# Optimization experiments

Hardware: AMD Instinct MI355X
Metric: run time of the kernel (lower is better)

## Reference

```python
import jax, jax.numpy as jnp
import numpy as np

NUM_HEAD = 16
HEAD_DIM = 64
SEQ, BATCH, DMODEL = 2048, 2, 1024


def setup_inputs() -> dict:
    key = jax.random.key(0)
    ks = jax.random.split(key, 6)
    xavier = lambda k, shp: jax.random.uniform(
        k, shp, jnp.float32, -1.0, 1.0) * np.sqrt(6.0 / (shp[0] + shp[1]))
    query = jax.random.normal(ks[0], (SEQ, BATCH, DMODEL), jnp.float32)
    q_w = xavier(ks[1], (DMODEL, DMODEL))
    k_w = xavier(ks[2], (DMODEL, DMODEL))
    v_w = xavier(ks[3], (DMODEL, DMODEL))
    out_w = xavier(ks[4], (DMODEL, DMODEL))
    zeros = jnp.zeros((DMODEL,), jnp.float32)
    # causal mask: True = masked out (key position after query position)
    causal = jnp.triu(jnp.ones((SEQ, SEQ), bool), k=1)
    attn_mask = jnp.broadcast_to(causal, (BATCH, SEQ, SEQ))
    return {
        "query": query,
        "q_w": q_w, "q_b": zeros,
        "k_w": k_w, "k_b": zeros,
        "v_w": v_w, "v_b": zeros,
        "out_w": out_w, "out_b": zeros,
        "attn_mask": attn_mask,
    }


def reference(query, q_w, q_b, k_w, k_b, v_w, v_b, out_w, out_b, attn_mask):
    S, B, _ = query.shape
    H, Dh = NUM_HEAD, HEAD_DIM
    scale = 1.0 / np.sqrt(Dh)
    # self-attention: key = value = query
    q = (query @ q_w.T + q_b).reshape(S, B, H, Dh)
    k = (query @ k_w.T + k_b).reshape(S, B, H, Dh)
    v = (query @ v_w.T + v_b).reshape(S, B, H, Dh)
    # scores: [B, H, S(query), S(key)]
    scores = jnp.einsum('sbhd,tbhd->bhst', q, k) * scale
    scores = jnp.where(attn_mask[:, None, :, :], -jnp.inf, scores)
    attn = jax.nn.softmax(scores, axis=-1)
    # context: [S, B, H, Dh] -> [S, B, H*Dh]
    ctx = jnp.einsum('bhst,tbhd->sbhd', attn, v).reshape(S, B, H * Dh)
    return ctx @ out_w.T + out_b
```

## Files before the change

kernel.cpp:

```cpp
#include <hip/hip_runtime.h>
#include <hip/hip_bf16.h>

typedef __bf16 bf16;
typedef __attribute__((ext_vector_type(2))) __bf16 bf16x2;
typedef __attribute__((ext_vector_type(4))) __bf16 bf16x4;
typedef __attribute__((ext_vector_type(8))) __bf16 bf16x8;
typedef __attribute__((ext_vector_type(4))) float f32x4;

static_assert(sizeof(bf16x8) == 16, "bf16x8 must be 16B");

#define S_LEN 2048
#define BATCH_N 2
#define DM 1024
#define NHEAD 16
#define HDIM 64
#define LOG2E 1.44269504088896f

__device__ __forceinline__ void async_cp16(const void* g, void* l) {
    __builtin_amdgcn_global_load_lds(
        (const __attribute__((address_space(1))) void*)g,
        (__attribute__((address_space(3))) void*)l, 16, 0, 0);
}

__global__ __launch_bounds__(256)
void cvt_all(const float* __restrict__ q,
             const float* __restrict__ w0, const float* __restrict__ w1,
             const float* __restrict__ w2, const float* __restrict__ w3,
             bf16* __restrict__ Xb,
             bf16* __restrict__ W0, bf16* __restrict__ W1,
             bf16* __restrict__ W2, bf16* __restrict__ W3) {
    const int blk = blockIdx.x;
    const float* src;
    bf16* dst;
    size_t base;
    if (blk < 2048) {
        src = q; dst = Xb; base = (size_t)blk * 2048;
    } else {
        const int w = (blk - 2048) >> 9;
        const int r = (blk - 2048) & 511;
        base = (size_t)r * 2048;
        src = (w == 0) ? w0 : (w == 1) ? w1 : (w == 2) ? w2 : w3;
        dst = (w == 0) ? W0 : (w == 1) ? W1 : (w == 2) ? W2 : W3;
    }
    const size_t i = base + (size_t)threadIdx.x * 8;
    const f32x4 a = *(const f32x4*)(src + i);
    const f32x4 b = *(const f32x4*)(src + i + 4);
    bf16x8 r8;
    r8[0] = (bf16)a[0]; r8[1] = (bf16)a[1]; r8[2] = (bf16)a[2]; r8[3] = (bf16)a[3];
    r8[4] = (bf16)b[0]; r8[5] = (bf16)b[1]; r8[6] = (bf16)b[2]; r8[7] = (bf16)b[3];
    *(bf16x8*)(dst + i) = r8;
}

__device__ __forceinline__ void gemm_tile(const bf16* __restrict__ A,
                                          const bf16* __restrict__ W,
                                          int row0, int col0, int Kdim,
                                          f32x4 acc[4][4]) {
    __shared__ bf16 As[128 * 32];
    __shared__ bf16 Bs[128 * 32];
    const int tid  = threadIdx.x;
    const int lane = tid & 63;
    const int wv   = tid >> 6;
    const int wr = wv >> 1, wc = wv & 1;
    const int qr = lane & 15, quad = lane >> 4;

    const int srow = wv * 16 + (lane >> 2);
    const int scol = (lane & 3) * 8;
    const bf16* Ap = A + (size_t)(row0 + srow) * Kdim + scol;
    const bf16* Wp = W + (size_t)(col0 + srow) * Kdim + scol;
    bf16* lA0 = As + wv * 512;
    bf16* lA1 = As + 64 * 32 + wv * 512;
    bf16* lB0 = Bs + wv * 512;
    bf16* lB1 = Bs + 64 * 32 + wv * 512;

    const f32x4 fzero = {0.f, 0.f, 0.f, 0.f};
    #pragma unroll
    for (int mi = 0; mi < 4; ++mi)
        #pragma unroll
        for (int ni = 0; ni < 4; ++ni)
            acc[mi][ni] = fzero;

    for (int k0 = 0; k0 < Kdim; k0 += 32) {
        __syncthreads();
        async_cp16(Ap + k0, lA0);
        async_cp16(Ap + (size_t)64 * Kdim + k0, lA1);
        async_cp16(Wp + k0, lB0);
        async_cp16(Wp + (size_t)64 * Kdim + k0, lB1);
        __syncthreads();

        bf16x8 af[4], bfr[4];
        #pragma unroll
        for (int mi = 0; mi < 4; ++mi)
            af[mi] = *(const bf16x8*)(As + (wr * 64 + mi * 16 + qr) * 32 + quad * 8);
        #pragma unroll
        for (int ni = 0; ni < 4; ++ni)
            bfr[ni] = *(const bf16x8*)(Bs + (wc * 64 + ni * 16 + qr) * 32 + quad * 8);
        #pragma unroll
        for (int mi = 0; mi < 4; ++mi)
            #pragma unroll
            for (int ni = 0; ni < 4; ++ni)
                acc[mi][ni] = __builtin_amdgcn_mfma_f32_16x16x32_bf16(
                    af[mi], bfr[ni], acc[mi][ni], 0, 0, 0);
    }
}

__global__ __launch_bounds__(256)
void qkv_kernel(const bf16* __restrict__ X,
                const bf16* __restrict__ Wq, const float* __restrict__ bq,
                const bf16* __restrict__ Wk, const float* __restrict__ bk,
                const bf16* __restrict__ Wv, const float* __restrict__ bv,
                bf16* __restrict__ Q, bf16* __restrict__ Kt, bf16* __restrict__ Vt) {
    const int mat  = blockIdx.z;
    const bf16*  W    = (mat == 0) ? Wq : (mat == 1) ? Wk : Wv;
    const float* bias = (mat == 0) ? bq : (mat == 1) ? bk : bv;
    const int col0 = blockIdx.x * 128;
    const int row0 = blockIdx.y * 128;

    f32x4 acc[4][4];
    gemm_tile(X, W, row0, col0, DM, acc);

    const int lane = threadIdx.x & 63;
    const int wave = threadIdx.x >> 6;
    const int wr = wave >> 1, wc = wave & 1;
    const int qr = lane & 15, quad = lane >> 4;

    #pragma unroll
    for (int ni = 0; ni < 4; ++ni) {
        const int n  = col0 + wc * 64 + ni * 16 + qr;
        const float bn = bias[n];
        const int h = n >> 6, dh = n & 63;
        #pragma unroll
        for (int mi = 0; mi < 4; ++mi) {
            const int i0 = row0 + wr * 64 + mi * 16 + quad * 4;
            const float v0 = acc[mi][ni][0] + bn;
            const float v1 = acc[mi][ni][1] + bn;
            const float v2 = acc[mi][ni][2] + bn;
            const float v3 = acc[mi][ni][3] + bn;
            if (mat == 2) {
                const int s0 = i0 >> 1;
                bf16x2 e0 = {(bf16)v0, (bf16)v2};
                bf16x2 e1 = {(bf16)v1, (bf16)v3};
                *(bf16x2*)(Vt + ((size_t)h * HDIM + dh) * S_LEN + s0) = e0;
                *(bf16x2*)(Vt + ((size_t)(NHEAD + h) * HDIM + dh) * S_LEN + s0) = e1;
            } else {
                #pragma unroll
                for (int r = 0; r < 4; ++r) {
                    const int i = i0 + r;
                    const int s = i >> 1, b = i & 1;
                    const float v = (r == 0) ? v0 : (r == 1) ? v1 : (r == 2) ? v2 : v3;
                    if (mat == 0) {
                        Q[((size_t)(b * NHEAD + h) * S_LEN + s) * HDIM + dh] =
                            (bf16)(v * (0.125f * LOG2E));
                    } else {
                        Kt[((size_t)(b * NHEAD + h) * S_LEN + s) * HDIM + dh] = (bf16)v;
                    }
                }
            }
        }
    }
}

#define PLD 40
#define PT  640

#define MFMA(a, b, c) __builtin_amdgcn_mfma_f32_16x16x32_bf16(a, b, c, 0, 0, 0)
#define EX(x) __builtin_amdgcn_exp2f(x)

__global__ __launch_bounds__(256)
void attn_part(const bf16* __restrict__ Q, const bf16* __restrict__ K,
               const bf16* __restrict__ Vt, bf16* __restrict__ ctx) {
    __shared__ __align__(16) char smem[21504];
    const int tid  = threadIdx.x;
    const int lane = tid & 63;
    const int wave = tid >> 6;
    const int qr = lane & 15, quad = lane >> 4;
    const int bh = blockIdx.x & 31;
    const int bx = blockIdx.x >> 5;
    const int b = bh >> 4, h = bh & 15;

    const char* Kg = (const char*)(K  + (size_t)bh * S_LEN * HDIM);
    const char* Vg = (const char*)(Vt + (size_t)bh * HDIM * S_LEN);
    const bf16* Qb = Q + (size_t)bh * S_LEN * HDIM;
    char* Ksm = smem;
    char* Vsm = smem + 8192;
    bf16* Pw  = (bf16*)(smem + 16384) + wave * PT;
    const f32x4 fzero = {0.f, 0.f, 0.f, 0.f};

    const int qb     = 31 - bx;
    const int qb0    = qb * 64;
    const int tdiag  = qb * 2;
    const int ntiles = 2 * qb + 2;

    const int d16   = tid * 16;
    const int ksrow = d16 >> 7;
    const int ksoff = (d16 & 127) ^ ((ksrow & 7) << 4);
    const int vsrow = d16 >> 6;
    const int vsoff = (d16 & 63) ^ ((vsrow & 3) << 4);
    const size_t kgbase = (size_t)ksrow * 128 + ksoff;
    const size_t vgbase = (size_t)vsrow * (S_LEN * 2) + vsoff;

#define STAGE(t_, bi_) do { \
    async_cp16(Kg + (size_t)(t_) * 4096 + kgbase, Ksm + (bi_) * 4096 + wave * 1024); \
    async_cp16(Vg + (size_t)(t_) * 64   + vgbase, Vsm + (bi_) * 4096 + wave * 1024); \
} while (0)

    const int qrow0 = qb0 + wave * 16;
    const bf16x8 qlo = *(const bf16x8*)(Qb + (size_t)(qrow0 + qr) * HDIM + quad * 8);
    const bf16x8 qhi = *(const bf16x8*)(Qb + (size_t)(qrow0 + qr) * HDIM + quad * 8 + 32);

    f32x4 o0 = fzero, o1 = fzero, o2 = fzero, o3 = fzero;
    float l = 0.f;

    STAGE(0, 0);
    __syncthreads();

    const int sK = (qr & 7) << 4;
    const int sV = (qr & 3) << 4;

    for (int t = 0; t < ntiles; ++t) {
        const int cur = t & 1;
        if (t + 1 < ntiles) STAGE(t + 1, cur ^ 1);

        const char* Kc = Ksm + cur * 4096;
        const char* Vc = Vsm + cur * 4096;
        const bf16x8 k0 = *(const bf16x8*)(Kc + qr * 128        + ((quad * 16)      ^ sK));
        const bf16x8 k1 = *(const bf16x8*)(Kc + qr * 128        + ((quad * 16 + 64) ^ sK));
        const bf16x8 k2 = *(const bf16x8*)(Kc + (16 + qr) * 128 + ((quad * 16)      ^ sK));
        const bf16x8 k3 = *(const bf16x8*)(Kc + (16 + qr) * 128 + ((quad * 16 + 64) ^ sK));
        const bf16x8 v0 = *(const bf16x8*)(Vc + qr * 64         + ((quad * 16) ^ sV));
        const bf16x8 v1 = *(const bf16x8*)(Vc + (16 + qr) * 64  + ((quad * 16) ^ sV));
        const bf16x8 v2 = *(const bf16x8*)(Vc + (32 + qr) * 64  + ((quad * 16) ^ sV));
        const bf16x8 v3 = *(const bf16x8*)(Vc + (48 + qr) * 64  + ((quad * 16) ^ sV));

        f32x4 sA = MFMA(k0, qlo, fzero); sA = MFMA(k1, qhi, sA);
        f32x4 sB = MFMA(k2, qlo, fzero); sB = MFMA(k3, qhi, sB);

        if (t < tdiag) {
            const float e0 = EX(sA[0]), e1 = EX(sA[1]), e2 = EX(sA[2]), e3 = EX(sA[3]);
            const float f0 = EX(sB[0]), f1 = EX(sB[1]), f2 = EX(sB[2]), f3 = EX(sB[3]);
            l += (e0 + e1 + e2 + e3) + (f0 + f1 + f2 + f3);
            bf16x4 wa = {(bf16)e0, (bf16)e1, (bf16)e2, (bf16)e3};
            bf16x4 wb = {(bf16)f0, (bf16)f1, (bf16)f2, (bf16)f3};
            *(bf16x4*)(Pw + qr * PLD + quad * 4)      = wa;
            *(bf16x4*)(Pw + qr * PLD + 16 + quad * 4) = wb;
        } else {
            const int qrow = qrow0 + qr;
            const int ka = t * 32 + quad * 4;
            const float e0 = (ka + 0  <= qrow) ? EX(sA[0]) : 0.f;
            const float e1 = (ka + 1  <= qrow) ? EX(sA[1]) : 0.f;
            const float e2 = (ka + 2  <= qrow) ? EX(sA[2]) : 0.f;
            const float e3 = (ka + 3  <= qrow) ? EX(sA[3]) : 0.f;
            const float f0 = (ka + 16 <= qrow) ? EX(sB[0]) : 0.f;
            const float f1 = (ka + 17 <= qrow) ? EX(sB[1]) : 0.f;
            const float f2 = (ka + 18 <= qrow) ? EX(sB[2]) : 0.f;
            const float f3 = (ka + 19 <= qrow) ? EX(sB[3]) : 0.f;
            l += (e0 + e1 + e2 + e3) + (f0 + f1 + f2 + f3);
            bf16x4 wa = {(bf16)e0, (bf16)e1, (bf16)e2, (bf16)e3};
            bf16x4 wb = {(bf16)f0, (bf16)f1, (bf16)f2, (bf16)f3};
            *(bf16x4*)(Pw + qr * PLD + quad * 4)      = wa;
            *(bf16x4*)(Pw + qr * PLD + 16 + quad * 4) = wb;
        }

        const bf16x8 pf = *(const bf16x8*)(Pw + qr * PLD + quad * 8);
        __builtin_amdgcn_s_setprio(1);
        o0 = MFMA(v0, pf, o0); o1 = MFMA(v1, pf, o1);
        o2 = MFMA(v2, pf, o2); o3 = MFMA(v3, pf, o3);
        __builtin_amdgcn_s_setprio(0);

        __syncthreads();
    }
#undef STAGE

    l += __shfl_xor(l, 16); l += __shfl_xor(l, 32);
    const float n = 1.f / l;

    const int s_ = qrow0 + qr;
    bf16* cp = ctx + ((size_t)s_ * BATCH_N + b) * DM + h * HDIM + quad * 4;
    #define CW(ov, vi_) do { \
        bf16x4 cc = {(bf16)(ov[0] * n), (bf16)(ov[1] * n), \
                     (bf16)(ov[2] * n), (bf16)(ov[3] * n)}; \
        *(bf16x4*)(cp + (vi_) * 16) = cc; \
    } while (0)
    CW(o0, 0); CW(o1, 1); CW(o2, 2); CW(o3, 3);
    #undef CW
}

__global__ __launch_bounds__(256)
void proj_kernel(const bf16* __restrict__ X, const bf16* __restrict__ W,
                 const float* __restrict__ bias, float* __restrict__ out) {
    const int col0 = blockIdx.x * 128;
    const int row0 = blockIdx.y * 128;
    f32x4 acc[4][4];
    gemm_tile(X, W, row0, col0, DM, acc);

    const int lane = threadIdx.x & 63;
    const int wave = threadIdx.x >> 6;
    const int wr = wave >> 1, wc = wave & 1;
    const int qr = lane & 15, quad = lane >> 4;

    #pragma unroll
    for (int ni = 0; ni < 4; ++ni) {
        const int n = col0 + wc * 64 + ni * 16 + qr;
        const float bn = bias[n];
        #pragma unroll
        for (int mi = 0; mi < 4; ++mi) {
            #pragma unroll
            for (int r = 0; r < 4; ++r) {
                const int i = row0 + wr * 64 + mi * 16 + quad * 4 + r;
                out[(size_t)i * DM + n] = acc[mi][ni][r] + bn;
            }
        }
    }
}

extern "C" void kernel_launch(void* const* d_in, const int* in_sizes, int n_in,
                              void* d_out, int out_size, void* d_ws, size_t ws_size,
                              hipStream_t stream) {
    (void)in_sizes; (void)n_in; (void)out_size; (void)ws_size;
    const float* query = (const float*)d_in[0];
    const float* q_w   = (const float*)d_in[1];
    const float* q_b   = (const float*)d_in[2];
    const float* k_w   = (const float*)d_in[3];
    const float* k_b   = (const float*)d_in[4];
    const float* v_w   = (const float*)d_in[5];
    const float* v_b   = (const float*)d_in[6];
    const float* out_w = (const float*)d_in[7];
    const float* out_b = (const float*)d_in[8];

    char* ws = (char*)d_ws;
    bf16*  Qb   = (bf16*)(ws);
    bf16*  Kb   = (bf16*)(ws + ((size_t)8  << 20));
    bf16*  Vt   = (bf16*)(ws + ((size_t)16 << 20));
    bf16*  ctx  = (bf16*)(ws + ((size_t)24 << 20));
    bf16*  Wob  = (bf16*)(ws + ((size_t)32 << 20));
    bf16*  Xb   = (bf16*)(ws + ((size_t)34 << 20));
    bf16*  Wqb  = (bf16*)(ws + ((size_t)42 << 20));
    bf16*  Wkb  = (bf16*)(ws + ((size_t)44 << 20));
    bf16*  Wvb  = (bf16*)(ws + ((size_t)46 << 20));
    float* out  = (float*)d_out;

    dim3 blk(256);
    cvt_all<<<dim3(2048 + 4 * 512), blk, 0, stream>>>(
        query, q_w, k_w, v_w, out_w, Xb, Wqb, Wkb, Wvb, Wob);

    qkv_kernel<<<dim3(DM / 128, (S_LEN * BATCH_N) / 128, 3), blk, 0, stream>>>(
        Xb, Wqb, q_b, Wkb, k_b, Wvb, v_b, Qb, Kb, Vt);
    attn_part<<<dim3(1024), blk, 0, stream>>>(Qb, Kb, Vt, ctx);
    proj_kernel<<<dim3(DM / 128, (S_LEN * BATCH_N) / 128), blk, 0, stream>>>(
        ctx, Wob, out_b, out);
}
```

Baseline: 207.3 us.

## Stage V transpose through LDS and halve attention block to 128 threads

The V projection epilogue now writes its tile into shared memory and then emits coalesced 16-byte rows into the transposed Vt layout, replacing scattered 4-byte stores. The attention kernel shrinks to two waves per block covering 32 query rows, doubles the grid to 2048 blocks, and issues two async copies per thread per operand to fill the same K/V tiles. The intent is cheaper global stores in the QKV kernel and finer-grained causal load balancing with more resident blocks. It adds two block barriers to the V epilogue and gives each attention block fewer waves to share each staged tile.

```diff
diff --git a/kernel.cpp b/kernel.cpp
--- a/kernel.cpp
+++ b/kernel.cpp
@@ -109,6 +109,7 @@
                 const bf16* __restrict__ Wk, const float* __restrict__ bk,
                 const bf16* __restrict__ Wv, const float* __restrict__ bv,
                 bf16* __restrict__ Q, bf16* __restrict__ Kt, bf16* __restrict__ Vt) {
+    __shared__ __align__(16) char vbuf[64 * 272];
     const int mat  = blockIdx.z;
     const bf16*  W    = (mat == 0) ? Wq : (mat == 1) ? Wk : Wv;
     const float* bias = (mat == 0) ? bq : (mat == 1) ? bk : bv;
@@ -118,10 +119,54 @@
     f32x4 acc[4][4];
     gemm_tile(X, W, row0, col0, DM, acc);
 
-    const int lane = threadIdx.x & 63;
-    const int wave = threadIdx.x >> 6;
+    const int tid  = threadIdx.x;
+    const int lane = tid & 63;
+    const int wave = tid >> 6;
     const int wr = wave >> 1, wc = wave & 1;
     const int qr = lane & 15, quad = lane >> 4;
+
+    if (mat == 2) {
+        const int s_half = row0 >> 1;
+        #pragma unroll
+        for (int w = 0; w < 2; ++w) {
+            __syncthreads();
+            if (wc == w) {
+                #pragma unroll
+                for (int ni = 0; ni < 4; ++ni) {
+                    const int n  = col0 + w * 64 + ni * 16 + qr;
+                    const float bn = bias[n];
+                    const int nl = ni * 16 + qr;
+                    #pragma unroll
+                    for (int mi = 0; mi < 4; ++mi) {
+                        const int i0 = wr * 64 + mi * 16 + quad * 4;
+                        const float v0 = acc[mi][ni][0] + bn;
+                        const float v1 = acc[mi][ni][1] + bn;
+                        const float v2 = acc[mi][ni][2] + bn;
+                        const float v3 = acc[mi][ni][3] + bn;
+                        bf16x2 e0 = {(bf16)v0, (bf16)v2};
+                        bf16x2 e1 = {(bf16)v1, (bf16)v3};
+                        *(bf16x2*)(vbuf + nl * 272 + i0)       = e0;
+                        *(bf16x2*)(vbuf + nl * 272 + 128 + i0) = e1;
+                    }
+                }
+            }
+            __syncthreads();
+            {
+                const int nl = tid >> 2;
+                const int b_ = (tid >> 1) & 1;
+                const int hf = tid & 1;
+                const int n  = col0 + w * 64 + nl;
+                const int hh = n >> 6, dd = n & 63;
+                const bf16* src = (const bf16*)(vbuf + nl * 272 + b_ * 128 + hf * 64);
+                bf16* dst = Vt + ((size_t)(b_ * NHEAD + hh) * 64 + dd) * 2048
+                               + s_half + hf * 32;
+                #pragma unroll
+                for (int c = 0; c < 4; ++c)
+                    *(bf16x8*)(dst + c * 8) = *(const bf16x8*)(src + c * 8);
+            }
+        }
+        return;
+    }
 
     #pragma unroll
     for (int ni = 0; ni < 4; ++ni) {
@@ -131,28 +176,16 @@
         #pragma unroll
         for (int mi = 0; mi < 4; ++mi) {
             const int i0 = row0 + wr * 64 + mi * 16 + quad * 4;
-            const float v0 = acc[mi][ni][0] + bn;
-            const float v1 = acc[mi][ni][1] + bn;
-            const float v2 = acc[mi][ni][2] + bn;
-            const float v3 = acc[mi][ni][3] + bn;
-            if (mat == 2) {
-                const int s0 = i0 >> 1;
-                bf16x2 e0 = {(bf16)v0, (bf16)v2};
-                bf16x2 e1 = {(bf16)v1, (bf16)v3};
-                *(bf16x2*)(Vt + ((size_t)h * HDIM + dh) * S_LEN + s0) = e0;
-                *(bf16x2*)(Vt + ((size_t)(NHEAD + h) * HDIM + dh) * S_LEN + s0) = e1;
-            } else {
-                #pragma unroll
-                for (int r = 0; r < 4; ++r) {
-                    const int i = i0 + r;
-                    const int s = i >> 1, b = i & 1;
-                    const float v = (r == 0) ? v0 : (r == 1) ? v1 : (r == 2) ? v2 : v3;
-                    if (mat == 0) {
-                        Q[((size_t)(b * NHEAD + h) * S_LEN + s) * HDIM + dh] =
-                            (bf16)(v * (0.125f * LOG2E));
-                    } else {
-                        Kt[((size_t)(b * NHEAD + h) * S_LEN + s) * HDIM + dh] = (bf16)v;
-                    }
+            #pragma unroll
+            for (int r = 0; r < 4; ++r) {
+                const int i = i0 + r;
+                const int s = i >> 1, b = i & 1;
+                const float v = acc[mi][ni][r] + bn;
+                if (mat == 0) {
+                    Q[((size_t)(b * NHEAD + h) * S_LEN + s) * HDIM + dh] =
+                        (bf16)(v * (0.125f * LOG2E));
+                } else {
+                    Kt[((size_t)(b * NHEAD + h) * S_LEN + s) * HDIM + dh] = (bf16)v;
                 }
             }
         }
@@ -165,16 +198,16 @@
 #define MFMA(a, b, c) __builtin_amdgcn_mfma_f32_16x16x32_bf16(a, b, c, 0, 0, 0)
 #define EX(x) __builtin_amdgcn_exp2f(x)
 
-__global__ __launch_bounds__(256)
+__global__ __launch_bounds__(128)
 void attn_part(const bf16* __restrict__ Q, const bf16* __restrict__ K,
                const bf16* __restrict__ Vt, bf16* __restrict__ ctx) {
-    __shared__ __align__(16) char smem[21504];
+    __shared__ __align__(16) char smem[18944];
     const int tid  = threadIdx.x;
     const int lane = tid & 63;
     const int wave = tid >> 6;
     const int qr = lane & 15, quad = lane >> 4;
     const int bh = blockIdx.x & 31;
-    const int bx = blockIdx.x >> 5;
+    const int qh = 63 - (int)(blockIdx.x >> 5);
     const int b = bh >> 4, h = bh & 15;
 
     const char* Kg = (const char*)(K  + (size_t)bh * S_LEN * HDIM);
@@ -185,25 +218,24 @@
     bf16* Pw  = (bf16*)(smem + 16384) + wave * PT;
     const f32x4 fzero = {0.f, 0.f, 0.f, 0.f};
 
-    const int qb     = 31 - bx;
-    const int qb0    = qb * 64;
-    const int tdiag  = qb * 2;
-    const int ntiles = 2 * qb + 2;
+    const int ntiles = qh + 1;
 
     const int d16   = tid * 16;
     const int ksrow = d16 >> 7;
     const int ksoff = (d16 & 127) ^ ((ksrow & 7) << 4);
+    const size_t kgbase = (size_t)ksrow * 128 + ksoff;
     const int vsrow = d16 >> 6;
     const int vsoff = (d16 & 63) ^ ((vsrow & 3) << 4);
-    const size_t kgbase = (size_t)ksrow * 128 + ksoff;
     const size_t vgbase = (size_t)vsrow * (S_LEN * 2) + vsoff;
 
 #define STAGE(t_, bi_) do { \
-    async_cp16(Kg + (size_t)(t_) * 4096 + kgbase, Ksm + (bi_) * 4096 + wave * 1024); \
-    async_cp16(Vg + (size_t)(t_) * 64   + vgbase, Vsm + (bi_) * 4096 + wave * 1024); \
+    async_cp16(Kg + (size_t)(t_) * 4096 + kgbase,        Ksm + (bi_) * 4096 + wave * 1024); \
+    async_cp16(Kg + (size_t)(t_) * 4096 + 2048 + kgbase, Ksm + (bi_) * 4096 + 2048 + wave * 1024); \
+    async_cp16(Vg + (size_t)(t_) * 64 + vgbase,          Vsm + (bi_) * 4096 + wave * 1024); \
+    async_cp16(Vg + (size_t)(t_) * 64 + 131072 + vgbase, Vsm + (bi_) * 4096 + 2048 + wave * 1024); \
 } while (0)
 
-    const int qrow0 = qb0 + wave * 16;
+    const int qrow0 = qh * 32 + wave * 16;
     const bf16x8 qlo = *(const bf16x8*)(Qb + (size_t)(qrow0 + qr) * HDIM + quad * 8);
     const bf16x8 qhi = *(const bf16x8*)(Qb + (size_t)(qrow0 + qr) * HDIM + quad * 8 + 32);
 
@@ -234,7 +266,7 @@
         f32x4 sA = MFMA(k0, qlo, fzero); sA = MFMA(k1, qhi, sA);
         f32x4 sB = MFMA(k2, qlo, fzero); sB = MFMA(k3, qhi, sB);
 
-        if (t < tdiag) {
+        if (t < qh) {
             const float e0 = EX(sA[0]), e1 = EX(sA[1]), e2 = EX(sA[2]), e3 = EX(sA[3]);
             const float f0 = EX(sB[0]), f1 = EX(sB[1]), f2 = EX(sB[2]), f3 = EX(sB[3]);
             l += (e0 + e1 + e2 + e3) + (f0 + f1 + f2 + f3);
@@ -344,7 +376,7 @@
 
     qkv_kernel<<<dim3(DM / 128, (S_LEN * BATCH_N) / 128, 3), blk, 0, stream>>>(
         Xb, Wqb, q_b, Wkb, k_b, Wvb, v_b, Qb, Kb, Vt);
-    attn_part<<<dim3(1024), blk, 0, stream>>>(Qb, Kb, Vt, ctx);
+    attn_part<<<dim3(2048), dim3(128), 0, stream>>>(Qb, Kb, Vt, ctx);
     proj_kernel<<<dim3(DM / 128, (S_LEN * BATCH_N) / 128), blk, 0, stream>>>(
         ctx, Wob, out_b, out);
 }
```

New measurement: 226.2 us. 9.1% more time.
